# Kernel optimization log

Measured on AMD Instinct MI355X. Metric: run time of the kernel, lower is better.

Reference implementation:

```python
import jax, jax.numpy as jnp
import numpy as np

B = 128        # batch (images/texts)
N = 2048       # other texts per image
F_IMG = 1024   # raw image feature dim (abstracted encoder input)
F_TXT = 512    # raw text feature dim
D = 512        # embedding dim (num_features=512 in BasicNet)
TOPK = B - 1   # default topK = batch - 1


def setup_inputs() -> dict:
    key = jax.random.key(0)
    ks = jax.random.split(key, 6)
    return {
        "input_images": jax.random.normal(ks[0], (B, F_IMG), jnp.float32),
        "input_texts": jax.random.normal(ks[1], (B, F_TXT), jnp.float32),
        "other_texts": jax.random.normal(ks[2], (B, N, F_TXT), jnp.float32),
        "W_img": jax.random.normal(ks[3], (F_IMG, D), jnp.float32) / np.float32(np.sqrt(F_IMG)),
        "W_txt": jax.random.normal(ks[4], (F_TXT, D), jnp.float32) / np.float32(np.sqrt(F_TXT)),
        "logit_scale": jnp.asarray(np.log(1.0 / 0.07), jnp.float32),
    }


def reference(input_images, input_texts, other_texts, W_img, W_txt, logit_scale):
    K = TOPK
    # encoders abstracted as linear projections to D=512
    img = input_images @ W_img                                   # [B, D]
    img = img / jnp.linalg.norm(img, axis=1, keepdims=True)      # L2-normalize images
    txt = input_texts @ W_txt                                    # [B, D]
    txt = txt / jnp.linalg.norm(txt, axis=1, keepdims=True)      # row-wise norm == norm after concat
    oth = jnp.einsum('bnf,fd->bnd', other_texts, W_txt)          # [B, N, D]
    oth = oth / jnp.linalg.norm(oth, axis=2, keepdims=True)

    scale = jnp.exp(logit_scale)
    logit_in = scale * jnp.sum(img * txt, axis=1)                # [B] image_i . text_i
    logit_oth = scale * jnp.einsum('bd,bnd->bn', img, oth)       # [B, N]

    # descending sort + take top-K (lax.top_k returns sorted descending)
    topk_vals, _ = jax.lax.top_k(logit_oth, K)                   # [B, K]

    # indices = sorted(range(K) + [min(i, K-1)]): duplicate element p=min(i,K-1)
    rows = jnp.arange(B)
    cols = jnp.arange(K + 1)[None, :]                            # [1, K+1]
    p = jnp.minimum(rows, K - 1)[:, None]                        # [B, 1]
    gidx = jnp.where(cols <= p, cols, cols - 1)                  # [B, K+1]
    gathered = jnp.take_along_axis(topk_vals, gidx, axis=1)      # [B, K+1]

    # overwrite column i of row i with the positive (input text) logit
    out = jnp.where(cols == rows[:, None], logit_in[:, None], gathered)
    return out
```

## Files before the change

### kernel.cpp

```cpp
#include <hip/hip_runtime.h>
#include <hip/hip_bf16.h>
#include <math.h>

#define B_SZ 128
#define N_OTH 2048
#define F_IMG 1024
#define F_TXT 512
#define D_EMB 512

typedef __attribute__((ext_vector_type(8))) short short8;
typedef __attribute__((ext_vector_type(16))) float f32x16;

static __device__ __forceinline__ ushort f2bf(float f) {
    __hip_bfloat16 h = __float2bfloat16(f);
    return *reinterpret_cast<ushort*>(&h);
}

__global__ __launch_bounds__(512) void k_prep(const float* __restrict__ in_img,
                                              const float* __restrict__ in_txt,
                                              const float* __restrict__ W_img,
                                              const float* __restrict__ W_txt,
                                              const float* __restrict__ p_ls,
                                              float* __restrict__ img,
                                              float* __restrict__ logit_in,
                                              ushort* __restrict__ wf) {
    if (blockIdx.x >= B_SZ) {
        const int g = (blockIdx.x - B_SZ) * 512 + threadIdx.x;
        const int l = g & 63;
        const int frag = g >> 6;
        const int kstep = frag >> 4;
        const int ct = frag & 15;
        const int col = ct * 32 + (l & 31);
        const int kb = kstep * 16 + (l >> 5) * 8;
        short8 o;
#pragma unroll
        for (int j = 0; j < 8; ++j) o[j] = (short)f2bf(W_txt[(kb + j) * D_EMB + col]);
        *(short8*)(wf + (size_t)g * 8) = o;
        return;
    }
    const int b = blockIdx.x;
    const int d = threadIdx.x;
    __shared__ float row[F_IMG];
    __shared__ float wsum[8];
    __shared__ float s_rn;
    const int lane = d & 63, wv = d >> 6;

    for (int i = d; i < F_IMG; i += 512) row[i] = in_img[b * F_IMG + i];
    __syncthreads();
    float acc = 0.f;
#pragma unroll 8
    for (int f = 0; f < F_IMG; ++f) acc = fmaf(row[f], W_img[f * D_EMB + d], acc);
    float sq = acc * acc;
#pragma unroll
    for (int off = 32; off > 0; off >>= 1) sq += __shfl_down(sq, off);
    if (lane == 0) wsum[wv] = sq;
    __syncthreads();
    if (d == 0) {
        float s = 0.f;
        for (int w = 0; w < 8; ++w) s += wsum[w];
        s_rn = 1.0f / sqrtf(s);
    }
    __syncthreads();
    const float iv = acc * s_rn;
    img[b * D_EMB + d] = iv;

    __syncthreads();
    row[d] = in_txt[b * F_TXT + d];
    __syncthreads();
    float tacc = 0.f;
#pragma unroll 8
    for (int f = 0; f < F_TXT; ++f) tacc = fmaf(row[f], W_txt[f * D_EMB + d], tacc);
    float tsq = tacc * tacc;
#pragma unroll
    for (int off = 32; off > 0; off >>= 1) tsq += __shfl_down(tsq, off);
    __syncthreads();
    if (lane == 0) wsum[wv] = tsq;
    __syncthreads();
    if (d == 0) {
        float s = 0.f;
        for (int w = 0; w < 8; ++w) s += wsum[w];
        s_rn = 1.0f / sqrtf(s);
    }
    __syncthreads();
    float pd = (tacc * s_rn) * iv;
#pragma unroll
    for (int off = 32; off > 0; off >>= 1) pd += __shfl_down(pd, off);
    __syncthreads();
    if (lane == 0) wsum[wv] = pd;
    __syncthreads();
    if (d == 0) {
        float s = 0.f;
        for (int w = 0; w < 8; ++w) s += wsum[w];
        logit_in[b] = expf(p_ls[0]) * s;
    }
}

__device__ __forceinline__ void loadA(const float* gs, float4 v[4]) {
    v[0] = *(const float4*)(gs + 0);
    v[1] = *(const float4*)(gs + 4);
    v[2] = *(const float4*)(gs + 8);
    v[3] = *(const float4*)(gs + 12);
}
__device__ __forceinline__ void cvtWrite(char* buf, int wb0, int wb1, const float4 v[4]) {
    short8 p0, p1;
    p0[0] = (short)f2bf(v[0].x); p0[1] = (short)f2bf(v[0].y); p0[2] = (short)f2bf(v[0].z); p0[3] = (short)f2bf(v[0].w);
    p0[4] = (short)f2bf(v[1].x); p0[5] = (short)f2bf(v[1].y); p0[6] = (short)f2bf(v[1].z); p0[7] = (short)f2bf(v[1].w);
    p1[0] = (short)f2bf(v[2].x); p1[1] = (short)f2bf(v[2].y); p1[2] = (short)f2bf(v[2].z); p1[3] = (short)f2bf(v[2].w);
    p1[4] = (short)f2bf(v[3].x); p1[5] = (short)f2bf(v[3].y); p1[6] = (short)f2bf(v[3].z); p1[7] = (short)f2bf(v[3].w);
    *(short8*)(buf + wb0) = p0;
    *(short8*)(buf + wb1) = p1;
}

__global__ __launch_bounds__(256, 2) void k_gemm(const float* __restrict__ oth,
                                                 const ushort* __restrict__ wf,
                                                 const float* __restrict__ img,
                                                 float* __restrict__ numA,
                                                 float* __restrict__ denA) {
    __shared__ ushort sA[3][64 * 64];
    __shared__ float redN[4][64];
    __shared__ float redD[4][64];
    const int tid = threadIdx.x;
    const int l = tid & 63;
    const int wv = tid >> 6;
    const int b = blockIdx.x >> 5;
    const size_t row0 = (size_t)blockIdx.x * 64;

    const int srow = tid >> 2;
    const int sk0 = (tid & 3) * 16;
    const float* gsrc = oth + (row0 + srow) * F_TXT + sk0;
    const int swz = (srow & 7) << 4;
    const int wb0 = srow * 128 + ((sk0 * 2 + 0) ^ swz);
    const int wb1 = srow * 128 + ((sk0 * 2 + 16) ^ swz);

    const ushort* wbase = wf + ((size_t)(wv * 4) * 64 + l) * 8;

    int rowbase[2];
#pragma unroll
    for (int m = 0; m < 2; ++m) rowbase[m] = (m * 32 + (l & 31)) * 128;
    int koff[4];
#pragma unroll
    for (int ks = 0; ks < 4; ++ks) koff[ks] = ((ks * 32 + (l >> 5) * 16) ^ ((l & 7) << 4));

    f32x16 acc[2][4];
#pragma unroll
    for (int m = 0; m < 2; ++m)
#pragma unroll
        for (int n = 0; n < 4; ++n)
#pragma unroll
            for (int r = 0; r < 16; ++r) acc[m][n][r] = 0.f;

    float4 va[4], vb[4];
    loadA(gsrc + 0 * 64, va);
    loadA(gsrc + 1 * 64, vb);
    __builtin_amdgcn_sched_barrier(0);
    cvtWrite((char*)sA[0], wb0, wb1, va);
    asm volatile("s_waitcnt lgkmcnt(0)" ::: "memory");
    __builtin_amdgcn_sched_barrier(0);
    __builtin_amdgcn_s_barrier();
    __builtin_amdgcn_sched_barrier(0);

#pragma unroll
    for (int t = 0; t < 8; ++t) {
        short8 bfr[4][4];
#pragma unroll
        for (int ks = 0; ks < 4; ++ks) {
            const ushort* bptr = wbase + (size_t)(t * 4 + ks) * 8192;
#pragma unroll
            for (int n = 0; n < 4; ++n)
                bfr[ks][n] = *(const short8*)(bptr + n * 512);
        }
        __builtin_amdgcn_sched_barrier(0);
        if (t < 6) {
            if ((t & 1) == 0) loadA(gsrc + (t + 2) * 64, va);
            else              loadA(gsrc + (t + 2) * 64, vb);
        }
        __builtin_amdgcn_sched_barrier(0);
        __builtin_amdgcn_s_setprio(1);
#pragma unroll
        for (int ks = 0; ks < 4; ++ks) {
            short8 af[2];
#pragma unroll
            for (int m = 0; m < 2; ++m)
                af[m] = *(const short8*)((const char*)sA[t % 3] + rowbase[m] + koff[ks]);
#pragma unroll
            for (int m = 0; m < 2; ++m)
#pragma unroll
                for (int n = 0; n < 4; ++n)
                    acc[m][n] = __builtin_amdgcn_mfma_f32_32x32x16_bf16(af[m], bfr[ks][n], acc[m][n], 0, 0, 0);
        }
        __builtin_amdgcn_s_setprio(0);
        if (t < 7) {
            if ((t & 1) == 0) cvtWrite((char*)sA[(t + 1) % 3], wb0, wb1, vb);
            else              cvtWrite((char*)sA[(t + 1) % 3], wb0, wb1, va);
        }
        asm volatile("s_waitcnt lgkmcnt(0)" ::: "memory");
        __builtin_amdgcn_sched_barrier(0);
        __builtin_amdgcn_s_barrier();
        __builtin_amdgcn_sched_barrier(0);
    }

    float ic[4];
#pragma unroll
    for (int n = 0; n < 4; ++n)
        ic[n] = img[b * D_EMB + wv * 128 + n * 32 + (l & 31)];
#pragma unroll
    for (int m = 0; m < 2; ++m) {
#pragma unroll
        for (int rg = 0; rg < 16; ++rg) {
            float tn = 0.f, td = 0.f;
#pragma unroll
            for (int n = 0; n < 4; ++n) {
                const float p = acc[m][n][rg];
                tn = fmaf(p, ic[n], tn);
                td = fmaf(p, p, td);
            }
#pragma unroll
            for (int off = 1; off <= 16; off <<= 1) {
                tn += __shfl_xor(tn, off);
                td += __shfl_xor(td, off);
            }
            if ((l & 31) == 0) {
                const int r = m * 32 + (rg & 3) + 8 * (rg >> 2) + 4 * (l >> 5);
                redN[wv][r] = tn;
                redD[wv][r] = td;
            }
        }
    }
    __syncthreads();
    if (tid < 64) {
        float tn = 0.f, td = 0.f;
#pragma unroll
        for (int w = 0; w < 4; ++w) { tn += redN[w][tid]; td += redD[w][tid]; }
        numA[row0 + tid] = tn;
        denA[row0 + tid] = td;
    }
}

__global__ __launch_bounds__(512) void k_topk(const float* __restrict__ numA,
                                              const float* __restrict__ denA,
                                              const float* __restrict__ logit_in,
                                              const float* __restrict__ p_ls,
                                              float* __restrict__ out) {
    const int b = blockIdx.x;
    const int tid = threadIdx.x;
    const float scale = expf(p_ls[0]);
    __shared__ float a[N_OTH];
    for (int i = tid; i < N_OTH; i += 512) {
        const float nu = numA[(size_t)b * N_OTH + i];
        const float de = denA[(size_t)b * N_OTH + i];
        a[i] = scale * nu / sqrtf(de);
    }
    __syncthreads();
    for (unsigned k = 2; k <= N_OTH; k <<= 1) {
        for (unsigned j = k >> 1; j > 0; j >>= 1) {
#pragma unroll
            for (int s = 0; s < N_OTH / 512; ++s) {
                const unsigned i = tid + s * 512u;
                const unsigned ixj = i ^ j;
                if (ixj > i) {
                    const bool asc = ((i & k) == 0);
                    const float x = a[i], y = a[ixj];
                    if ((x > y) == asc) { a[i] = y; a[ixj] = x; }
                }
            }
            __syncthreads();
        }
    }
    if (tid < 128) {
        const int j = tid;
        float v;
        if (j == b) {
            v = logit_in[b];
        } else {
            const int m = j - (j > b ? 1 : 0);
            v = a[N_OTH - 1 - m];
        }
        out[b * 128 + j] = v;
    }
}

extern "C" void kernel_launch(void* const* d_in, const int* in_sizes, int n_in,
                              void* d_out, int out_size, void* d_ws, size_t ws_size,
                              hipStream_t stream) {
    const float* in_img = (const float*)d_in[0];
    const float* in_txt = (const float*)d_in[1];
    const float* oth    = (const float*)d_in[2];
    const float* W_img  = (const float*)d_in[3];
    const float* W_txt  = (const float*)d_in[4];
    const float* p_ls   = (const float*)d_in[5];
    float* out = (float*)d_out;

    float* ws = (float*)d_ws;
    float* img      = ws;
    float* logit_in = ws + 65536;
    float* numA     = ws + 65536 + 128;
    float* denA     = numA + 262144;
    ushort* wfrag   = (ushort*)(denA + 262144);

    k_prep<<<B_SZ + 64, 512, 0, stream>>>(in_img, in_txt, W_img, W_txt, p_ls, img, logit_in, wfrag);
    k_gemm<<<(B_SZ * N_OTH) / 64, 256, 0, stream>>>(oth, wfrag, img, numA, denA);
    k_topk<<<B_SZ, 512, 0, stream>>>(numA, denA, logit_in, p_ls, out);
}
```

Baseline: 337.8 us.

## Enlarge GEMM block tile to 128 rows with 8 waves and double buffering

The projection-and-score GEMM now gives each block 128 rows of other_texts and 512 threads. Each of the 8 waves owns a 128x64 output slice, so every weight fragment loaded into registers is reused across four M tiles instead of two, which halves weight-fragment traffic per row. The shared-memory A buffer moves from three stages to two, and the A prefetch distance drops from two k-tiles to one. Weight fragments for the next k-tile are now loaded after the MFMA block, overlapping with the conversion write. The risks are less latency hiding on the dominant fp32 global stream and half as many blocks in the grid.

Result: slower. 399.9 us (+18.4%).

```diff
diff --git a/kernel.cpp b/kernel.cpp
--- a/kernel.cpp
+++ b/kernel.cpp
@@ -111,19 +111,19 @@
     *(short8*)(buf + wb1) = p1;
 }
 
-__global__ __launch_bounds__(256, 2) void k_gemm(const float* __restrict__ oth,
+__global__ __launch_bounds__(512, 2) void k_gemm(const float* __restrict__ oth,
                                                  const ushort* __restrict__ wf,
                                                  const float* __restrict__ img,
                                                  float* __restrict__ numA,
                                                  float* __restrict__ denA) {
-    __shared__ ushort sA[3][64 * 64];
-    __shared__ float redN[4][64];
-    __shared__ float redD[4][64];
+    __shared__ ushort sA[2][128 * 64];
+    __shared__ float redN[8][128];
+    __shared__ float redD[8][128];
     const int tid = threadIdx.x;
     const int l = tid & 63;
     const int wv = tid >> 6;
-    const int b = blockIdx.x >> 5;
-    const size_t row0 = (size_t)blockIdx.x * 64;
+    const int b = blockIdx.x >> 4;
+    const size_t row0 = (size_t)blockIdx.x * 128;
 
     const int srow = tid >> 2;
     const int sk0 = (tid & 3) * 16;
@@ -132,88 +132,78 @@
     const int wb0 = srow * 128 + ((sk0 * 2 + 0) ^ swz);
     const int wb1 = srow * 128 + ((sk0 * 2 + 16) ^ swz);
 
-    const ushort* wbase = wf + ((size_t)(wv * 4) * 64 + l) * 8;
-
-    int rowbase[2];
-#pragma unroll
-    for (int m = 0; m < 2; ++m) rowbase[m] = (m * 32 + (l & 31)) * 128;
+    int rowbase[4];
+#pragma unroll
+    for (int m = 0; m < 4; ++m) rowbase[m] = (m * 32 + (l & 31)) * 128;
     int koff[4];
 #pragma unroll
     for (int ks = 0; ks < 4; ++ks) koff[ks] = ((ks * 32 + (l >> 5) * 16) ^ ((l & 7) << 4));
 
-    f32x16 acc[2][4];
-#pragma unroll
-    for (int m = 0; m < 2; ++m)
-#pragma unroll
-        for (int n = 0; n < 4; ++n)
+    f32x16 acc[4][2];
+#pragma unroll
+    for (int m = 0; m < 4; ++m)
+#pragma unroll
+        for (int n = 0; n < 2; ++n)
 #pragma unroll
             for (int r = 0; r < 16; ++r) acc[m][n][r] = 0.f;
 
-    float4 va[4], vb[4];
-    loadA(gsrc + 0 * 64, va);
-    loadA(gsrc + 1 * 64, vb);
-    __builtin_amdgcn_sched_barrier(0);
+    float4 va[4];
+    short8 bfr[4][2];
+
+    loadA(gsrc, va);
+#pragma unroll
+    for (int ks = 0; ks < 4; ++ks)
+#pragma unroll
+        for (int n = 0; n < 2; ++n)
+            bfr[ks][n] = *(const short8*)(wf + ((size_t)(ks * 16 + wv * 2 + n) * 64 + l) * 8);
     cvtWrite((char*)sA[0], wb0, wb1, va);
-    asm volatile("s_waitcnt lgkmcnt(0)" ::: "memory");
-    __builtin_amdgcn_sched_barrier(0);
-    __builtin_amdgcn_s_barrier();
-    __builtin_amdgcn_sched_barrier(0);
+    __syncthreads();
 
 #pragma unroll
     for (int t = 0; t < 8; ++t) {
-        short8 bfr[4][4];
-#pragma unroll
-        for (int ks = 0; ks < 4; ++ks) {
-            const ushort* bptr = wbase + (size_t)(t * 4 + ks) * 8192;
-#pragma unroll
-            for (int n = 0; n < 4; ++n)
-                bfr[ks][n] = *(const short8*)(bptr + n * 512);
-        }
-        __builtin_amdgcn_sched_barrier(0);
-        if (t < 6) {
-            if ((t & 1) == 0) loadA(gsrc + (t + 2) * 64, va);
-            else              loadA(gsrc + (t + 2) * 64, vb);
-        }
+        const int cur = t & 1;
+        if (t < 7) loadA(gsrc + (t + 1) * 64, va);
         __builtin_amdgcn_sched_barrier(0);
         __builtin_amdgcn_s_setprio(1);
 #pragma unroll
         for (int ks = 0; ks < 4; ++ks) {
-            short8 af[2];
-#pragma unroll
-            for (int m = 0; m < 2; ++m)
-                af[m] = *(const short8*)((const char*)sA[t % 3] + rowbase[m] + koff[ks]);
-#pragma unroll
-            for (int m = 0; m < 2; ++m)
-#pragma unroll
-                for (int n = 0; n < 4; ++n)
+            short8 af[4];
+#pragma unroll
+            for (int m = 0; m < 4; ++m)
+                af[m] = *(const short8*)((const char*)sA[cur] + rowbase[m] + koff[ks]);
+#pragma unroll
+            for (int m = 0; m < 4; ++m)
+#pragma unroll
+                for (int n = 0; n < 2; ++n)
                     acc[m][n] = __builtin_amdgcn_mfma_f32_32x32x16_bf16(af[m], bfr[ks][n], acc[m][n], 0, 0, 0);
         }
         __builtin_amdgcn_s_setprio(0);
+        __builtin_amdgcn_sched_barrier(0);
         if (t < 7) {
-            if ((t & 1) == 0) cvtWrite((char*)sA[(t + 1) % 3], wb0, wb1, vb);
-            else              cvtWrite((char*)sA[(t + 1) % 3], wb0, wb1, va);
-        }
-        asm volatile("s_waitcnt lgkmcnt(0)" ::: "memory");
-        __builtin_amdgcn_sched_barrier(0);
-        __builtin_amdgcn_s_barrier();
-        __builtin_amdgcn_sched_barrier(0);
-    }
-
-    float ic[4];
-#pragma unroll
-    for (int n = 0; n < 4; ++n)
-        ic[n] = img[b * D_EMB + wv * 128 + n * 32 + (l & 31)];
-#pragma unroll
-    for (int m = 0; m < 2; ++m) {
+#pragma unroll
+            for (int ks = 0; ks < 4; ++ks)
+#pragma unroll
+                for (int n = 0; n < 2; ++n)
+                    bfr[ks][n] = *(const short8*)(wf + ((size_t)((t + 1) * 64 + ks * 16 + wv * 2 + n) * 64 + l) * 8);
+            __builtin_amdgcn_sched_barrier(0);
+            cvtWrite((char*)sA[cur ^ 1], wb0, wb1, va);
+            asm volatile("s_waitcnt lgkmcnt(0)" ::: "memory");
+            __builtin_amdgcn_sched_barrier(0);
+            __builtin_amdgcn_s_barrier();
+            __builtin_amdgcn_sched_barrier(0);
+        }
+    }
+
+    const float ic0 = img[b * D_EMB + wv * 64 + (l & 31)];
+    const float ic1 = img[b * D_EMB + wv * 64 + 32 + (l & 31)];
+#pragma unroll
+    for (int m = 0; m < 4; ++m) {
 #pragma unroll
         for (int rg = 0; rg < 16; ++rg) {
-            float tn = 0.f, td = 0.f;
-#pragma unroll
-            for (int n = 0; n < 4; ++n) {
-                const float p = acc[m][n][rg];
-                tn = fmaf(p, ic[n], tn);
-                td = fmaf(p, p, td);
-            }
+            const float p = acc[m][0][rg];
+            const float q = acc[m][1][rg];
+            float tn = p * ic0 + q * ic1;
+            float td = p * p + q * q;
 #pragma unroll
             for (int off = 1; off <= 16; off <<= 1) {
                 tn += __shfl_xor(tn, off);
@@ -227,10 +217,10 @@
         }
     }
     __syncthreads();
-    if (tid < 64) {
+    if (tid < 128) {
         float tn = 0.f, td = 0.f;
 #pragma unroll
-        for (int w = 0; w < 4; ++w) { tn += redN[w][tid]; td += redD[w][tid]; }
+        for (int w = 0; w < 8; ++w) { tn += redN[w][tid]; td += redD[w][tid]; }
         numA[row0 + tid] = tn;
         denA[row0 + tid] = td;
     }
@@ -298,6 +288,6 @@
     ushort* wfrag   = (ushort*)(denA + 262144);
 
     k_prep<<<B_SZ + 64, 512, 0, stream>>>(in_img, in_txt, W_img, W_txt, p_ls, img, logit_in, wfrag);
-    k_gemm<<<(B_SZ * N_OTH) / 64, 256, 0, stream>>>(oth, wfrag, img, numA, denA);
+    k_gemm<<<(B_SZ * N_OTH) / 128, 512, 0, stream>>>(oth, wfrag, img, numA, denA);
     k_topk<<<B_SZ, 512, 0, stream>>>(numA, denA, logit_in, p_ls, out);
 }
```

## Split GEMM N dimension across two blocks with double-buffered B fragments

Applied to the files above, without the earlier changes.

Each 64-row strip is now processed by two blocks, each computing half of the 512 output columns, and the partial numerator and denominator sums are written separately and added in the top-k kernel. Blocks are remapped so the two halves of a strip and neighbouring strips share the XCD for L2 reuse of the A rows. B fragments are prefetched one iteration ahead into registers, with fewer accumulators per wave. The cost is that A is read and converted twice and the workspace doubles, in exchange for more parallelism, less register pressure and better latency hiding.

Result: slower. 437.1 us (+29.4%).

```diff
diff --git a/kernel.cpp b/kernel.cpp
--- a/kernel.cpp
+++ b/kernel.cpp
@@ -7,6 +7,7 @@
 #define F_IMG 1024
 #define F_TXT 512
 #define D_EMB 512
+#define TOT (B_SZ * N_OTH)
 
 typedef __attribute__((ext_vector_type(8))) short short8;
 typedef __attribute__((ext_vector_type(16))) float f32x16;
@@ -101,6 +102,13 @@
     v[2] = *(const float4*)(gs + 8);
     v[3] = *(const float4*)(gs + 12);
 }
+__device__ __forceinline__ void loadB(short8 dst[4][2], const ushort* wbase, int t) {
+#pragma unroll
+    for (int ks = 0; ks < 4; ++ks)
+#pragma unroll
+        for (int n = 0; n < 2; ++n)
+            dst[ks][n] = *(const short8*)(wbase + (size_t)((t * 4 + ks) * 16 + n) * 512);
+}
 __device__ __forceinline__ void cvtWrite(char* buf, int wb0, int wb1, const float4 v[4]) {
     short8 p0, p1;
     p0[0] = (short)f2bf(v[0].x); p0[1] = (short)f2bf(v[0].y); p0[2] = (short)f2bf(v[0].z); p0[3] = (short)f2bf(v[0].w);
@@ -109,6 +117,21 @@
     p1[4] = (short)f2bf(v[3].x); p1[5] = (short)f2bf(v[3].y); p1[6] = (short)f2bf(v[3].z); p1[7] = (short)f2bf(v[3].w);
     *(short8*)(buf + wb0) = p0;
     *(short8*)(buf + wb1) = p1;
+}
+__device__ __forceinline__ void tileMFMA(const ushort* sAt, const int rowbase[2], const int koff[4],
+                                         const short8 bfr[4][2], f32x16 acc[2][2]) {
+#pragma unroll
+    for (int ks = 0; ks < 4; ++ks) {
+        short8 af[2];
+#pragma unroll
+        for (int m = 0; m < 2; ++m)
+            af[m] = *(const short8*)((const char*)sAt + rowbase[m] + koff[ks]);
+#pragma unroll
+        for (int m = 0; m < 2; ++m)
+#pragma unroll
+            for (int n = 0; n < 2; ++n)
+                acc[m][n] = __builtin_amdgcn_mfma_f32_32x32x16_bf16(af[m], bfr[ks][n], acc[m][n], 0, 0, 0);
+    }
 }
 
 __global__ __launch_bounds__(256, 2) void k_gemm(const float* __restrict__ oth,
@@ -122,8 +145,13 @@
     const int tid = threadIdx.x;
     const int l = tid & 63;
     const int wv = tid >> 6;
-    const int b = blockIdx.x >> 5;
-    const size_t row0 = (size_t)blockIdx.x * 64;
+    const int raw = blockIdx.x;
+    const int x = raw & 7;
+    const int q = raw >> 3;
+    const int strip = x * 512 + (q >> 1);
+    const int h = q & 1;
+    const int b = strip >> 5;
+    const size_t row0 = (size_t)strip * 64;
 
     const int srow = tid >> 2;
     const int sk0 = (tid & 3) * 16;
@@ -132,7 +160,7 @@
     const int wb0 = srow * 128 + ((sk0 * 2 + 0) ^ swz);
     const int wb1 = srow * 128 + ((sk0 * 2 + 16) ^ swz);
 
-    const ushort* wbase = wf + ((size_t)(wv * 4) * 64 + l) * 8;
+    const ushort* wbase = wf + ((size_t)(h * 8 + wv * 2) * 64 + l) * 8;
 
     int rowbase[2];
 #pragma unroll
@@ -141,17 +169,20 @@
 #pragma unroll
     for (int ks = 0; ks < 4; ++ks) koff[ks] = ((ks * 32 + (l >> 5) * 16) ^ ((l & 7) << 4));
 
-    f32x16 acc[2][4];
+    f32x16 acc[2][2];
 #pragma unroll
     for (int m = 0; m < 2; ++m)
 #pragma unroll
-        for (int n = 0; n < 4; ++n)
+        for (int n = 0; n < 2; ++n)
 #pragma unroll
             for (int r = 0; r < 16; ++r) acc[m][n][r] = 0.f;
 
     float4 va[4], vb[4];
+    short8 bfrA[4][2], bfrB[4][2];
+
     loadA(gsrc + 0 * 64, va);
     loadA(gsrc + 1 * 64, vb);
+    loadB(bfrA, wbase, 0);
     __builtin_amdgcn_sched_barrier(0);
     cvtWrite((char*)sA[0], wb0, wb1, va);
     asm volatile("s_waitcnt lgkmcnt(0)" ::: "memory");
@@ -161,13 +192,9 @@
 
 #pragma unroll
     for (int t = 0; t < 8; ++t) {
-        short8 bfr[4][4];
-#pragma unroll
-        for (int ks = 0; ks < 4; ++ks) {
-            const ushort* bptr = wbase + (size_t)(t * 4 + ks) * 8192;
-#pragma unroll
-            for (int n = 0; n < 4; ++n)
-                bfr[ks][n] = *(const short8*)(bptr + n * 512);
+        if (t < 7) {
+            if ((t & 1) == 0) loadB(bfrB, wbase, t + 1);
+            else              loadB(bfrA, wbase, t + 1);
         }
         __builtin_amdgcn_sched_barrier(0);
         if (t < 6) {
@@ -176,44 +203,34 @@
         }
         __builtin_amdgcn_sched_barrier(0);
         __builtin_amdgcn_s_setprio(1);
-#pragma unroll
-        for (int ks = 0; ks < 4; ++ks) {
-            short8 af[2];
-#pragma unroll
-            for (int m = 0; m < 2; ++m)
-                af[m] = *(const short8*)((const char*)sA[t % 3] + rowbase[m] + koff[ks]);
-#pragma unroll
-            for (int m = 0; m < 2; ++m)
-#pragma unroll
-                for (int n = 0; n < 4; ++n)
-                    acc[m][n] = __builtin_amdgcn_mfma_f32_32x32x16_bf16(af[m], bfr[ks][n], acc[m][n], 0, 0, 0);
-        }
+        if ((t & 1) == 0) tileMFMA(sA[t % 3], rowbase, koff, bfrA, acc);
+        else              tileMFMA(sA[t % 3], rowbase, koff, bfrB, acc);
         __builtin_amdgcn_s_setprio(0);
+        __builtin_amdgcn_sched_barrier(0);
         if (t < 7) {
             if ((t & 1) == 0) cvtWrite((char*)sA[(t + 1) % 3], wb0, wb1, vb);
             else              cvtWrite((char*)sA[(t + 1) % 3], wb0, wb1, va);
         }
-        asm volatile("s_waitcnt lgkmcnt(0)" ::: "memory");
-        __builtin_amdgcn_sched_barrier(0);
-        __builtin_amdgcn_s_barrier();
-        __builtin_amdgcn_sched_barrier(0);
-    }
-
-    float ic[4];
-#pragma unroll
-    for (int n = 0; n < 4; ++n)
-        ic[n] = img[b * D_EMB + wv * 128 + n * 32 + (l & 31)];
+        if (t < 7) {
+            asm volatile("s_waitcnt lgkmcnt(0)" ::: "memory");
+            __builtin_amdgcn_sched_barrier(0);
+            __builtin_amdgcn_s_barrier();
+            __builtin_amdgcn_sched_barrier(0);
+        }
+    }
+
+    float ic[2];
+#pragma unroll
+    for (int n = 0; n < 2; ++n)
+        ic[n] = img[b * D_EMB + h * 256 + wv * 64 + n * 32 + (l & 31)];
 #pragma unroll
     for (int m = 0; m < 2; ++m) {
 #pragma unroll
         for (int rg = 0; rg < 16; ++rg) {
-            float tn = 0.f, td = 0.f;
-#pragma unroll
-            for (int n = 0; n < 4; ++n) {
-                const float p = acc[m][n][rg];
-                tn = fmaf(p, ic[n], tn);
-                td = fmaf(p, p, td);
-            }
+            const float p = acc[m][0][rg];
+            const float qv = acc[m][1][rg];
+            float tn = p * ic[0] + qv * ic[1];
+            float td = p * p + qv * qv;
 #pragma unroll
             for (int off = 1; off <= 16; off <<= 1) {
                 tn += __shfl_xor(tn, off);
@@ -231,8 +248,8 @@
         float tn = 0.f, td = 0.f;
 #pragma unroll
         for (int w = 0; w < 4; ++w) { tn += redN[w][tid]; td += redD[w][tid]; }
-        numA[row0 + tid] = tn;
-        denA[row0 + tid] = td;
+        numA[(size_t)h * TOT + row0 + tid] = tn;
+        denA[(size_t)h * TOT + row0 + tid] = td;
     }
 }
 
@@ -246,8 +263,9 @@
     const float scale = expf(p_ls[0]);
     __shared__ float a[N_OTH];
     for (int i = tid; i < N_OTH; i += 512) {
-        const float nu = numA[(size_t)b * N_OTH + i];
-        const float de = denA[(size_t)b * N_OTH + i];
+        const size_t idx = (size_t)b * N_OTH + i;
+        const float nu = numA[idx] + numA[TOT + idx];
+        const float de = denA[idx] + denA[TOT + idx];
         a[i] = scale * nu / sqrtf(de);
     }
     __syncthreads();
@@ -294,10 +312,10 @@
     float* img      = ws;
     float* logit_in = ws + 65536;
     float* numA     = ws + 65536 + 128;
-    float* denA     = numA + 262144;
-    ushort* wfrag   = (ushort*)(denA + 262144);
+    float* denA     = numA + 2 * TOT;
+    ushort* wfrag   = (ushort*)(denA + 2 * TOT);
 
     k_prep<<<B_SZ + 64, 512, 0, stream>>>(in_img, in_txt, W_img, W_txt, p_ls, img, logit_in, wfrag);
-    k_gemm<<<(B_SZ * N_OTH) / 64, 256, 0, stream>>>(oth, wfrag, img, numA, denA);
+    k_gemm<<<(TOT / 64) * 2, 256, 0, stream>>>(oth, wfrag, img, numA, denA);
     k_topk<<<B_SZ, 512, 0, stream>>>(numA, denA, logit_in, p_ls, out);
 }
```
